# Performance work log

Measured on AMD Instinct MI355X. Metric: run time of the kernel, lower is better.

Reference implementation:

```python
import jax, jax.numpy as jnp
import numpy as np
import math

B, S, E, H = 2, 4096, 1024, 16
W = 256  # one-sided attention window (attention_window // 2)


def setup_inputs() -> dict:
    key = jax.random.key(0)
    ks = jax.random.split(key, 7)
    init = lambda k, shp: jax.random.normal(k, shp, jnp.float32) * 0.02
    return {
        "hidden_states": jax.random.normal(ks[0], (B, S, E), jnp.float32),
        "attention_mask": jnp.zeros((B, S), jnp.int32),  # 0 = local attention
        "q_w": init(ks[1], (E, E)), "q_b": jnp.zeros((E,), jnp.float32),
        "k_w": init(ks[2], (E, E)), "k_b": jnp.zeros((E,), jnp.float32),
        "v_w": init(ks[3], (E, E)), "v_b": jnp.zeros((E,), jnp.float32),
    }


def _banded_attention(hidden_states, attention_mask, q_w, q_b, k_w, k_b, v_w, v_b):
    D = E // H          # head dim
    w = W               # one-sided window
    nc = S // w         # number of query chunks of length w
    # Projections (torch Linear: x @ W.T + b); query pre-scaled by sqrt(head_dim)
    q = (hidden_states @ q_w.T + q_b) / math.sqrt(D)
    k = hidden_states @ k_w.T + k_b
    v = hidden_states @ v_w.T + v_b
    heads = lambda x: x.reshape(B, S, H, D).transpose(0, 2, 1, 3)  # [B,H,S,D]
    q, k, v = heads(q), heads(k), heads(v)

    qc = q.reshape(B, H, nc, w, D)                       # [B,H,nc,w,D]
    pad = lambda x: jnp.pad(x, ((0, 0), (0, 0), (w, w), (0, 0)))
    # chunk c of keys/values covers padded positions [c*w, c*w + 3w)
    idx = (jnp.arange(nc) * w)[:, None] + jnp.arange(3 * w)[None, :]  # [nc,3w]
    kc = pad(k)[:, :, idx]                               # [B,H,nc,3w,D]
    vc = pad(v)[:, :, idx]                               # [B,H,nc,3w,D]

    # banded scores: query x in chunk attends padded key y; rel offset = y-w-x
    scores = jnp.einsum('bhcxd,bhcyd->bhcxy', qc, kc)    # [B,H,nc,w,3w]

    # additive mask from attention_mask (!=0 -> -10000 at that key position)
    fm = jnp.where(attention_mask != 0, -10000.0, 0.0)   # [B,S]
    fmc = jnp.pad(fm, ((0, 0), (w, w)))[:, idx]          # [B,nc,3w]
    scores = scores + fmc[:, None, :, None, :]

    # validity: |rel| <= w (the 2w+1 band) and key index j in [0, S)
    x = jnp.arange(w)[:, None]                           # [w,1]
    y = jnp.arange(3 * w)[None, :]                       # [1,3w]
    rel = y - w - x                                      # [w,3w]
    j = (jnp.arange(nc) * w)[:, None, None] + (y - w)[None]  # [nc,1,3w] key idx
    valid = (jnp.abs(rel) <= w)[None] & (j >= 0) & (j < S)   # [nc,w,3w]
    scores = jnp.where(valid[None, None], scores, -jnp.inf)

    probs = jax.nn.softmax(scores.astype(jnp.float32), axis=-1)
    ctx = jnp.einsum('bhcxy,bhcyd->bhcxd', probs, vc)    # [B,H,nc,w,D]
    return ctx.reshape(B, H, S, D).transpose(0, 2, 1, 3).reshape(B, S, E)


def reference(hidden_states, attention_mask, q_w, q_b, k_w, k_b, v_w, v_b):
    return _banded_attention(hidden_states, attention_mask,
                             q_w, q_b, k_w, k_b, v_w, v_b)
```

## Files before the change

### kernel.cpp

```cpp
#include <hip/hip_runtime.h>
#include <math.h>

constexpr int Bn  = 2;
constexpr int Sn  = 4096;
constexpr int En  = 1024;
constexpr int Hn  = 16;
constexpr int Mtot = Bn * Sn;
constexpr int Kp  = 1024;
constexpr int PAD = 72;

typedef __bf16    bf16x8 __attribute__((ext_vector_type(8)));
typedef __bf16    bf16x4 __attribute__((ext_vector_type(4)));
typedef _Float16  f16x8  __attribute__((ext_vector_type(8)));
typedef _Float16  f16x4  __attribute__((ext_vector_type(4)));
typedef float     f32x4  __attribute__((ext_vector_type(4)));

__global__ void __launch_bounds__(256)
cvt_hs_kernel(const float* __restrict__ hs, _Float16* __restrict__ hs16)
{
    int t = blockIdx.x * 256 + threadIdx.x;
    int m = t >> 8;
    int k = (t & 255) << 2;
    float4 x = *(const float4*)&hs[((size_t)m << 10) + k];
    f16x4 h;
    h[0] = (_Float16)x.x; h[1] = (_Float16)x.y;
    h[2] = (_Float16)x.z; h[3] = (_Float16)x.w;
    *(f16x4*)&hs16[((size_t)m << 10) + k] = h;
}

__global__ void __launch_bounds__(256)
cvt_w_kernel(const float* __restrict__ qw, const float* __restrict__ kw,
             const float* __restrict__ vw, _Float16* __restrict__ w16)
{
    int t = blockIdx.x * 256 + threadIdx.x;
    int gn = t >> 8;
    int k  = (t & 255) << 2;
    int p  = gn >> 10, n = gn & 1023;
    const float* src = (p == 0) ? qw : (p == 1) ? kw : vw;
    float4 x = *(const float4*)&src[((size_t)n << 10) + k];
    f16x4 h;
    h[0] = (_Float16)x.x; h[1] = (_Float16)x.y;
    h[2] = (_Float16)x.z; h[3] = (_Float16)x.w;
    *(f16x4*)&w16[((size_t)gn << 10) + k] = h;
}

__device__ inline void load_lds16(const void* g, void* s) {
    __builtin_amdgcn_global_load_lds((const __attribute__((address_space(1))) void*)g,
                                     (__attribute__((address_space(3))) void*)s,
                                     16, 0, 0);
}

__device__ inline void block_sync() {
    asm volatile("" ::: "memory");
    __builtin_amdgcn_s_barrier();
    asm volatile("" ::: "memory");
}
__device__ inline void block_sync_vm0() {
    asm volatile("s_waitcnt vmcnt(0)" ::: "memory");
    __builtin_amdgcn_s_barrier();
    asm volatile("" ::: "memory");
}

template<int PM>
__global__ void __launch_bounds__(512, 2)
qkv_mfma_kernel(const _Float16* __restrict__ A2, const _Float16* __restrict__ B2,
                const float* __restrict__ qb, const float* __restrict__ kb,
                const float* __restrict__ vb,
                __bf16* __restrict__ q16, __bf16* __restrict__ k16,
                __bf16* __restrict__ vt16, int n0base)
{
    __shared__ _Float16 As[2][256 * 64];
    __shared__ _Float16 Bs[2][256 * 64];

    const int tid  = threadIdx.x;
    const int w    = tid >> 6;
    const int lane = tid & 63;
    const int wm   = w >> 2, wn = w & 3;
    const int mrow = lane & 15, quad = lane >> 4;
    const int m0   = blockIdx.x * 256;
    const int n0   = n0base + blockIdx.y * 256;

    const int subrow = lane >> 3;
    const int g8     = ((lane & 7) ^ subrow) * 8;
    const _Float16* Ag = A2 + (size_t)(m0 + w * 32 + subrow) * Kp + g8;
    const _Float16* Bg = B2 + (size_t)(n0 + w * 32 + subrow) * Kp + g8;

    const int arow = wm * 128 + mrow;
    const int brow = wn * 64 + mrow;
    const int cx   = quad ^ (mrow & 7);

    f32x4 acc[8][4] = {};

    auto stageA = [&](int kt, int bi) {
        const int k0 = kt * 64;
#pragma unroll
        for (int l = 0; l < 4; l++)
            load_lds16(Ag + (size_t)l * 8 * Kp + k0, &As[bi][(w * 32 + l * 8) * 64]);
    };
    auto stageB = [&](int kt, int bi) {
        const int k0 = kt * 64;
#pragma unroll
        for (int l = 0; l < 4; l++)
            load_lds16(Bg + (size_t)l * 8 * Kp + k0, &Bs[bi][(w * 32 + l * 8) * 64]);
    };
    auto ladder = [&](const f16x8* AF, const f16x8* BF, int r0) {
        __builtin_amdgcn_s_setprio(1);
#pragma unroll
        for (int ti = 0; ti < 4; ti++)
#pragma unroll
            for (int tj = 0; tj < 4; tj++) {
                if (PM == 0)
                    acc[r0 + ti][tj] = __builtin_amdgcn_mfma_f32_16x16x32_f16(
                        BF[tj], AF[ti], acc[r0 + ti][tj], 0, 0, 0);
                else
                    acc[r0 + ti][tj] = __builtin_amdgcn_mfma_f32_16x16x32_f16(
                        AF[ti], BF[tj], acc[r0 + ti][tj], 0, 0, 0);
            }
        __builtin_amdgcn_s_setprio(0);
    };

    constexpr int NT = Kp / 64;

    stageA(0, 0);
    stageB(0, 0);
    block_sync_vm0();

    for (int kt = 0; kt < NT; ++kt) {
        const int rb = kt & 1, wb = rb ^ 1;
        const _Float16* AsR = &As[rb][0];
        const _Float16* BsR = &Bs[rb][0];
        f16x8 af[4], bf[4];

#pragma unroll
        for (int t = 0; t < 4; t++)
            af[t] = *(const f16x8*)&AsR[(arow + t * 16) * 64 + cx * 8];
#pragma unroll
        for (int t = 0; t < 4; t++)
            bf[t] = *(const f16x8*)&BsR[(brow + t * 16) * 64 + cx * 8];
        if (kt + 1 < NT) stageA(kt + 1, wb);
        block_sync();
        ladder(af, bf, 0);
        block_sync();

#pragma unroll
        for (int t = 0; t < 4; t++)
            af[t] = *(const f16x8*)&AsR[(arow + 64 + t * 16) * 64 + cx * 8];
        if (kt + 1 < NT) stageB(kt + 1, wb);
        block_sync();
        ladder(af, bf, 4);
        block_sync();

#pragma unroll
        for (int t = 0; t < 4; t++)
            af[t] = *(const f16x8*)&AsR[(arow + t * 16) * 64 + (cx ^ 4) * 8];
#pragma unroll
        for (int t = 0; t < 4; t++)
            bf[t] = *(const f16x8*)&BsR[(brow + t * 16) * 64 + (cx ^ 4) * 8];
        block_sync();
        ladder(af, bf, 0);
        block_sync();

#pragma unroll
        for (int t = 0; t < 4; t++)
            af[t] = *(const f16x8*)&AsR[(arow + 64 + t * 16) * 64 + (cx ^ 4) * 8];
        block_sync();
        ladder(af, bf, 4);
        block_sync_vm0();
    }

    if (PM == 0) {
        const int p = n0 >> 10;
        const float* bptr = (p == 0) ? qb : kb;
        __bf16* dst = (p == 0) ? q16 : k16;
        const float scl = (p == 0) ? 0.125f : 1.0f;
#pragma unroll
        for (int ti = 0; ti < 8; ti++) {
            const int m  = m0 + wm * 128 + ti * 16 + mrow;
            const int bb = m >> 12, ss = m & 4095;
#pragma unroll
            for (int tj = 0; tj < 4; tj++) {
                const int fl = (n0 + wn * 64 + tj * 16 + quad * 4) & 1023;
                const int hh = fl >> 6, dd = fl & 63;
                const float4 bv = *(const float4*)&bptr[fl];
                bf16x4 o;
                o[0] = (__bf16)((acc[ti][tj][0] + bv.x) * scl);
                o[1] = (__bf16)((acc[ti][tj][1] + bv.y) * scl);
                o[2] = (__bf16)((acc[ti][tj][2] + bv.z) * scl);
                o[3] = (__bf16)((acc[ti][tj][3] + bv.w) * scl);
                *(bf16x4*)&dst[((size_t)(bb * Hn + hh) * Sn + ss) * 64 + dd] = o;
            }
        }
    } else {
#pragma unroll
        for (int tj = 0; tj < 4; tj++) {
            const int n  = n0 + wn * 64 + tj * 16 + mrow;
            const float bv = vb[n & 1023];
            const int hh = (n & 1023) >> 6, dd = n & 63;
#pragma unroll
            for (int ti = 0; ti < 8; ti++) {
                const int m  = m0 + wm * 128 + ti * 16 + quad * 4;
                const int bb = m >> 12, ss = m & 4095;
                bf16x4 pv4;
#pragma unroll
                for (int r = 0; r < 4; r++)
                    pv4[r] = (__bf16)(acc[ti][tj][r] + bv);
                *(bf16x4*)&vt16[((size_t)(bb * Hn + hh) * 64 + dd) * Sn + ss] = pv4;
            }
        }
    }
}

__global__ void __launch_bounds__(256, 2)
banded_attn_kernel(const __bf16* __restrict__ q16, const __bf16* __restrict__ k16,
                   const __bf16* __restrict__ vt16, const int* __restrict__ mask,
                   float* __restrict__ out)
{
    __shared__ __bf16 Kt[2][64 * PAD];
    __shared__ __bf16 Vt[2][64 * PAD];
    __shared__ __bf16 Pt[4][64 * PAD];
    __shared__ float  Msh[768];

    const int c = blockIdx.x, h = blockIdx.y, b = blockIdx.z;
    const int bh = b * Hn + h;
    const int i0 = c * 256;
    const int jwin0 = i0 - 256;
    const int tid  = threadIdx.x;
    const int wv   = tid >> 6;
    const int lane = tid & 63;
    const int quad = lane >> 4, mrow = lane & 15;

#pragma unroll
    for (int rep = 0; rep < 3; rep++) {
        int idx = rep * 256 + tid;
        int jg  = jwin0 + idx;
        float mv = 0.f;
        if (jg >= 0 && jg < Sn && mask[b * Sn + jg] != 0) mv = -10000.f;
        Msh[idx] = mv;
    }

    bf16x8 qf[4][2];
    const __bf16* qbase = q16 + (((size_t)bh * Sn + i0 + wv * 64) << 6);
#pragma unroll
    for (int tjq = 0; tjq < 4; tjq++)
#pragma unroll
        for (int kc = 0; kc < 2; kc++)
            qf[tjq][kc] = *(const bf16x8*)(qbase + (16 * tjq + mrow) * 64 + 32 * kc + 8 * quad);

    const int sr = lane >> 3;
    const int sc = lane & 7;
    bf16x8 kreg0, kreg1, vreg0, vreg1;
    auto gload = [&](int st) {
        const int j0 = jwin0 + st * 64;
        const int r0 = wv * 16 + sr;
        const int r1 = wv * 16 + 8 + sr;
        int jk0 = j0 + r0; jk0 = jk0 < 0 ? 0 : (jk0 > Sn - 1 ? Sn - 1 : jk0);
        int jk1 = j0 + r1; jk1 = jk1 < 0 ? 0 : (jk1 > Sn - 1 ? Sn - 1 : jk1);
        kreg0 = *(const bf16x8*)&k16[(((size_t)bh * Sn + jk0) << 6) + sc * 8];
        kreg1 = *(const bf16x8*)&k16[(((size_t)bh * Sn + jk1) << 6) + sc * 8];
        int jv = j0 + sc * 8; jv = jv < 0 ? 0 : (jv > Sn - 8 ? Sn - 8 : jv);
        vreg0 = *(const bf16x8*)&vt16[((size_t)bh * 64 + r0) * Sn + jv];
        vreg1 = *(const bf16x8*)&vt16[((size_t)bh * 64 + r1) * Sn + jv];
    };
    auto swrite = [&](int buf) {
        *(bf16x8*)&Kt[buf][(wv * 16 + sr) * PAD + sc * 8]     = kreg0;
        *(bf16x8*)&Kt[buf][(wv * 16 + 8 + sr) * PAD + sc * 8] = kreg1;
        *(bf16x8*)&Vt[buf][(wv * 16 + sr) * PAD + sc * 8]     = vreg0;
        *(bf16x8*)&Vt[buf][(wv * 16 + 8 + sr) * PAD + sc * 8] = vreg1;
    };

    f32x4 acc_o[4][4] = {};
    float lrun[4] = {0.f, 0.f, 0.f, 0.f};
    __bf16* Pw = &Pt[wv][0];

    gload(0);
    swrite(0);
    __syncthreads();

    for (int st = 0; st < 12; st++) {
        const int buf = st & 1;
        if (st + 1 < 12) gload(st + 1);

        if (st >= wv && st <= wv + 8) {
            const __bf16* KtB = &Kt[buf][0];
            const __bf16* VtB = &Vt[buf][0];
#pragma unroll
            for (int ti = 0; ti < 4; ti++) {
                bf16x8 ak0 = *(const bf16x8*)&KtB[(16 * ti + mrow) * PAD + quad * 8];
                bf16x8 ak1 = *(const bf16x8*)&KtB[(16 * ti + mrow) * PAD + 32 + quad * 8];
                const int y0 = 64 * st + 16 * ti + 4 * quad;
                f32x4 ms4 = *(const f32x4*)&Msh[y0];
#pragma unroll
                for (int tjq = 0; tjq < 4; tjq++) {
                    f32x4 s = {};
                    s = __builtin_amdgcn_mfma_f32_16x16x32_bf16(ak0, qf[tjq][0], s, 0, 0, 0);
                    s = __builtin_amdgcn_mfma_f32_16x16x32_bf16(ak1, qf[tjq][1], s, 0, 0, 0);
                    const int xq = 64 * wv + 16 * tjq + mrow;
                    bf16x4 pk;
                    float psum = 0.f;
#pragma unroll
                    for (int r = 0; r < 4; r++) {
                        const int y = y0 + r;
                        bool ok = ((unsigned)(y - xq) <= 512u) &
                                  ((unsigned)(jwin0 + y) < 4096u);
                        float pv = ok ? __expf(s[r] + ms4[r]) : 0.f;
                        psum += pv;
                        pk[r] = (__bf16)pv;
                    }
                    lrun[tjq] += psum;
                    *(bf16x4*)&Pw[(16 * tjq + mrow) * PAD + 16 * ti + 4 * quad] = pk;
                }
            }
#pragma unroll
            for (int kc2 = 0; kc2 < 2; kc2++) {
                bf16x8 av[4];
#pragma unroll
                for (int dt = 0; dt < 4; dt++)
                    av[dt] = *(const bf16x8*)&VtB[(16 * dt + mrow) * PAD + kc2 * 32 + quad * 8];
#pragma unroll
                for (int tjq = 0; tjq < 4; tjq++) {
                    bf16x8 pf = *(const bf16x8*)&Pw[(16 * tjq + mrow) * PAD + kc2 * 32 + quad * 8];
#pragma unroll
                    for (int dt = 0; dt < 4; dt++)
                        acc_o[dt][tjq] = __builtin_amdgcn_mfma_f32_16x16x32_bf16(
                            av[dt], pf, acc_o[dt][tjq], 0, 0, 0);
                }
            }
        }

        if (st + 1 < 12) {
            swrite((st + 1) & 1);
            __syncthreads();
        }
    }

    float inv[4];
#pragma unroll
    for (int tjq = 0; tjq < 4; tjq++) {
        float l = lrun[tjq];
        l += __shfl_xor(l, 16);
        l += __shfl_xor(l, 32);
        inv[tjq] = 1.0f / l;
    }
#pragma unroll
    for (int dt = 0; dt < 4; dt++)
#pragma unroll
        for (int tjq = 0; tjq < 4; tjq++) {
            f32x4 o = acc_o[dt][tjq];
            o[0] *= inv[tjq]; o[1] *= inv[tjq]; o[2] *= inv[tjq]; o[3] *= inv[tjq];
            float* dst = out + ((size_t)(b * Sn + i0 + wv * 64 + 16 * tjq + mrow)) * En
                             + h * 64 + 16 * dt + 4 * quad;
            *(f32x4*)dst = o;
        }
}

extern "C" void kernel_launch(void* const* d_in, const int* in_sizes, int n_in,
                              void* d_out, int out_size, void* d_ws, size_t ws_size,
                              hipStream_t stream) {
    const float* hs  = (const float*)d_in[0];
    const int*  mask = (const int*)d_in[1];
    const float* qw  = (const float*)d_in[2];
    const float* qb  = (const float*)d_in[3];
    const float* kw  = (const float*)d_in[4];
    const float* kb  = (const float*)d_in[5];
    const float* vw  = (const float*)d_in[6];
    const float* vb  = (const float*)d_in[7];
    float* out = (float*)d_out;

    _Float16* hs16 = (_Float16*)d_ws;
    _Float16* w16  = (_Float16*)((char*)d_ws + (size_t)16777216);
    __bf16*   q16  = (__bf16*)((char*)d_ws + (size_t)23068672);
    __bf16*   k16  = (__bf16*)((char*)d_ws + (size_t)39845888);
    __bf16*   vt16 = (__bf16*)((char*)d_ws + (size_t)56623104);

    cvt_hs_kernel<<<8192, 256, 0, stream>>>(hs, hs16);
    cvt_w_kernel <<<3072, 256, 0, stream>>>(qw, kw, vw, w16);

    dim3 pgridQK(Mtot / 256, 2048 / 256);
    qkv_mfma_kernel<0><<<pgridQK, 512, 0, stream>>>(hs16, w16, qb, kb, vb,
                                                    q16, k16, vt16, 0);
    dim3 pgridV(Mtot / 256, 1024 / 256);
    qkv_mfma_kernel<1><<<pgridV, 512, 0, stream>>>(hs16, w16, qb, kb, vb,
                                                   q16, k16, vt16, 2048);

    dim3 agrid(Sn / 256, Hn, Bn);
    banded_attn_kernel<<<agrid, 256, 0, stream>>>(q16, k16, vt16, mask, out);
}
```

Measured before the change: 229.7 us.

## Split QKV GEMM K-tile into halves with partial vmcnt waits

Splits each 64-wide K tile of the QKV projection GEMM into two 32-wide LDS halves with a new swizzle. Each half is staged on its own, and `s_waitcnt vmcnt(8)` / `vmcnt(4)` replace the full `vmcnt(0)` drain, so MFMA work on one half can start while the other half's global-to-LDS loads are still in flight. Bias values are also loaded once before the main loop instead of in the epilogue. The cost is more fragile counter-based synchronisation, which depends on exact load counts, and a changed LDS bank-conflict pattern.

```diff
diff --git a/kernel.cpp b/kernel.cpp
--- a/kernel.cpp
+++ b/kernel.cpp
@@ -55,11 +55,9 @@
     __builtin_amdgcn_s_barrier();
     asm volatile("" ::: "memory");
 }
-__device__ inline void block_sync_vm0() {
-    asm volatile("s_waitcnt vmcnt(0)" ::: "memory");
-    __builtin_amdgcn_s_barrier();
-    asm volatile("" ::: "memory");
-}
+__device__ inline void vm_wait8() { asm volatile("s_waitcnt vmcnt(8)" ::: "memory"); }
+__device__ inline void vm_wait4() { asm volatile("s_waitcnt vmcnt(4)" ::: "memory"); }
+__device__ inline void vm_wait0() { asm volatile("s_waitcnt vmcnt(0)" ::: "memory"); }
 
 template<int PM>
 __global__ void __launch_bounds__(512, 2)
@@ -69,8 +67,8 @@
                 __bf16* __restrict__ q16, __bf16* __restrict__ k16,
                 __bf16* __restrict__ vt16, int n0base)
 {
-    __shared__ _Float16 As[2][256 * 64];
-    __shared__ _Float16 Bs[2][256 * 64];
+    __shared__ _Float16 As[2][2][256][32];
+    __shared__ _Float16 Bs[2][2][256][32];
 
     const int tid  = threadIdx.x;
     const int w    = tid >> 6;
@@ -80,28 +78,26 @@
     const int m0   = blockIdx.x * 256;
     const int n0   = n0base + blockIdx.y * 256;
 
-    const int subrow = lane >> 3;
-    const int g8     = ((lane & 7) ^ subrow) * 8;
-    const _Float16* Ag = A2 + (size_t)(m0 + w * 32 + subrow) * Kp + g8;
-    const _Float16* Bg = B2 + (size_t)(n0 + w * 32 + subrow) * Kp + g8;
-
-    const int arow = wm * 128 + mrow;
-    const int brow = wn * 64 + mrow;
-    const int cx   = quad ^ (mrow & 7);
+    const int subrow = lane >> 2;
+    const int gch    = ((lane & 3) ^ ((lane >> 3) & 3)) * 8;
+    const _Float16* Ag = A2 + (size_t)(m0 + w * 32 + subrow) * Kp + gch;
+    const _Float16* Bg = B2 + (size_t)(n0 + w * 32 + subrow) * Kp + gch;
+
+    const int sl = (quad ^ ((mrow >> 1) & 3)) * 8;
 
     f32x4 acc[8][4] = {};
 
-    auto stageA = [&](int kt, int bi) {
-        const int k0 = kt * 64;
-#pragma unroll
-        for (int l = 0; l < 4; l++)
-            load_lds16(Ag + (size_t)l * 8 * Kp + k0, &As[bi][(w * 32 + l * 8) * 64]);
-    };
-    auto stageB = [&](int kt, int bi) {
-        const int k0 = kt * 64;
-#pragma unroll
-        for (int l = 0; l < 4; l++)
-            load_lds16(Bg + (size_t)l * 8 * Kp + k0, &Bs[bi][(w * 32 + l * 8) * 64]);
+    auto stageA = [&](int kt, int bi, int kc) {
+        const size_t goff = (size_t)kt * 64 + kc * 32;
+#pragma unroll
+        for (int l = 0; l < 2; l++)
+            load_lds16(Ag + (size_t)l * 16 * Kp + goff, &As[bi][kc][w * 32 + l * 16][0]);
+    };
+    auto stageB = [&](int kt, int bi, int kc) {
+        const size_t goff = (size_t)kt * 64 + kc * 32;
+#pragma unroll
+        for (int l = 0; l < 2; l++)
+            load_lds16(Bg + (size_t)l * 16 * Kp + goff, &Bs[bi][kc][w * 32 + l * 16][0]);
     };
     auto ladder = [&](const f16x8* AF, const f16x8* BF, int r0) {
         __builtin_amdgcn_s_setprio(1);
@@ -121,56 +117,73 @@
 
     constexpr int NT = Kp / 64;
 
-    stageA(0, 0);
-    stageB(0, 0);
-    block_sync_vm0();
+    float4 bv4[4];
+    const int p = n0 >> 10;
+    {
+        const float* bptr = (p == 0) ? qb : (p == 1) ? kb : vb;
+#pragma unroll
+        for (int tj = 0; tj < 4; tj++) {
+            if (PM == 0) {
+                const int fl = (n0 + wn * 64 + tj * 16 + quad * 4) & 1023;
+                bv4[tj] = *(const float4*)&bptr[fl];
+            } else {
+                const int n = (n0 + wn * 64 + tj * 16 + mrow) & 1023;
+                bv4[tj].x = bptr[n];
+            }
+        }
+    }
+
+    stageA(0, 0, 0); stageB(0, 0, 0);
+    stageA(0, 0, 1); stageB(0, 0, 1);
+    vm_wait4();
+    block_sync();
 
     for (int kt = 0; kt < NT; ++kt) {
         const int rb = kt & 1, wb = rb ^ 1;
-        const _Float16* AsR = &As[rb][0];
-        const _Float16* BsR = &Bs[rb][0];
+        const bool pre  = (kt + 1 < NT);
+        const bool last = (kt + 1 == NT);
         f16x8 af[4], bf[4];
 
 #pragma unroll
         for (int t = 0; t < 4; t++)
-            af[t] = *(const f16x8*)&AsR[(arow + t * 16) * 64 + cx * 8];
-#pragma unroll
-        for (int t = 0; t < 4; t++)
-            bf[t] = *(const f16x8*)&BsR[(brow + t * 16) * 64 + cx * 8];
-        if (kt + 1 < NT) stageA(kt + 1, wb);
+            af[t] = *(const f16x8*)&As[rb][0][wm * 128 + t * 16 + mrow][sl];
+#pragma unroll
+        for (int t = 0; t < 4; t++)
+            bf[t] = *(const f16x8*)&Bs[rb][0][wn * 64 + t * 16 + mrow][sl];
+        if (pre) { stageA(kt + 1, wb, 0); stageB(kt + 1, wb, 0); }
         block_sync();
         ladder(af, bf, 0);
         block_sync();
 
 #pragma unroll
         for (int t = 0; t < 4; t++)
-            af[t] = *(const f16x8*)&AsR[(arow + 64 + t * 16) * 64 + cx * 8];
-        if (kt + 1 < NT) stageB(kt + 1, wb);
+            af[t] = *(const f16x8*)&As[rb][0][wm * 128 + 64 + t * 16 + mrow][sl];
+        if (pre) { stageA(kt + 1, wb, 1); stageB(kt + 1, wb, 1); }
         block_sync();
         ladder(af, bf, 4);
-        block_sync();
-
-#pragma unroll
-        for (int t = 0; t < 4; t++)
-            af[t] = *(const f16x8*)&AsR[(arow + t * 16) * 64 + (cx ^ 4) * 8];
-#pragma unroll
-        for (int t = 0; t < 4; t++)
-            bf[t] = *(const f16x8*)&BsR[(brow + t * 16) * 64 + (cx ^ 4) * 8];
+        if (last) vm_wait0(); else vm_wait8();
+        block_sync();
+
+#pragma unroll
+        for (int t = 0; t < 4; t++)
+            af[t] = *(const f16x8*)&As[rb][1][wm * 128 + t * 16 + mrow][sl];
+#pragma unroll
+        for (int t = 0; t < 4; t++)
+            bf[t] = *(const f16x8*)&Bs[rb][1][wn * 64 + t * 16 + mrow][sl];
         block_sync();
         ladder(af, bf, 0);
         block_sync();
 
 #pragma unroll
         for (int t = 0; t < 4; t++)
-            af[t] = *(const f16x8*)&AsR[(arow + 64 + t * 16) * 64 + (cx ^ 4) * 8];
+            af[t] = *(const f16x8*)&As[rb][1][wm * 128 + 64 + t * 16 + mrow][sl];
         block_sync();
         ladder(af, bf, 4);
-        block_sync_vm0();
+        vm_wait4();
+        block_sync();
     }
 
     if (PM == 0) {
-        const int p = n0 >> 10;
-        const float* bptr = (p == 0) ? qb : kb;
         __bf16* dst = (p == 0) ? q16 : k16;
         const float scl = (p == 0) ? 0.125f : 1.0f;
 #pragma unroll
@@ -181,12 +194,11 @@
             for (int tj = 0; tj < 4; tj++) {
                 const int fl = (n0 + wn * 64 + tj * 16 + quad * 4) & 1023;
                 const int hh = fl >> 6, dd = fl & 63;
-                const float4 bv = *(const float4*)&bptr[fl];
                 bf16x4 o;
-                o[0] = (__bf16)((acc[ti][tj][0] + bv.x) * scl);
-                o[1] = (__bf16)((acc[ti][tj][1] + bv.y) * scl);
-                o[2] = (__bf16)((acc[ti][tj][2] + bv.z) * scl);
-                o[3] = (__bf16)((acc[ti][tj][3] + bv.w) * scl);
+                o[0] = (__bf16)((acc[ti][tj][0] + bv4[tj].x) * scl);
+                o[1] = (__bf16)((acc[ti][tj][1] + bv4[tj].y) * scl);
+                o[2] = (__bf16)((acc[ti][tj][2] + bv4[tj].z) * scl);
+                o[3] = (__bf16)((acc[ti][tj][3] + bv4[tj].w) * scl);
                 *(bf16x4*)&dst[((size_t)(bb * Hn + hh) * Sn + ss) * 64 + dd] = o;
             }
         }
@@ -194,7 +206,7 @@
 #pragma unroll
         for (int tj = 0; tj < 4; tj++) {
             const int n  = n0 + wn * 64 + tj * 16 + mrow;
-            const float bv = vb[n & 1023];
+            const float bv = bv4[tj].x;
             const int hh = (n & 1023) >> 6, dd = n & 63;
 #pragma unroll
             for (int ti = 0; ti < 8; ti++) {
```

Result: faster. 225.0 us (-2.0%).
